# Kernel tuning notes

Measured on AMD Instinct MI355X. Metric: run time of the kernel, lower is better.

Reference implementation:

```python
import jax, jax.numpy as jnp
import numpy as np

B, L, D, H = 2, 2048, 1024, 16
LARGE_NEG = 10000.0
CLAMP = 20.0


def setup_inputs() -> dict:
    key = jax.random.key(0)
    ks = jax.random.split(key, 7)
    scale = 1.0 / np.sqrt(D)
    return {
        "x": jax.random.normal(ks[0], (B, L, D), dtype=jnp.float32),
        "key_padding_mask": jax.random.randint(ks[1], (B, L), 0, 2, dtype=jnp.int32),
        "attn_bias": jax.random.normal(ks[2], (B, H, L, L), dtype=jnp.float32),
        "W_in": jax.random.normal(ks[3], (3 * D, D), dtype=jnp.float32) * scale,
        "b_in": jnp.zeros((3 * D,), dtype=jnp.float32),
        "W_out": jax.random.normal(ks[4], (D, D), dtype=jnp.float32) * scale,
        "b_out": jnp.zeros((D,), dtype=jnp.float32),
    }


def reference(x, key_padding_mask, attn_bias, W_in, b_in, W_out, b_out):
    d = D // H
    # fused in-projection: [B,L,3D]
    qkv = x @ W_in.T + b_in
    q, k, v = jnp.split(qkv, 3, axis=-1)
    # [B,H,L,d]
    q = q.reshape(B, L, H, d).transpose(0, 2, 1, 3)
    k = k.reshape(B, L, H, d).transpose(0, 2, 1, 3)
    v = v.reshape(B, L, H, d).transpose(0, 2, 1, 3)
    scores = jnp.einsum("bhqd,bhkd->bhqk", q, k) / jnp.sqrt(jnp.float32(d))
    scores = scores + attn_bias
    # key padding: subtract large_neg where mask==1 (mask broadcast over heads, queries)
    pad = key_padding_mask.astype(scores.dtype)[:, None, None, :]
    scores = scores - LARGE_NEG * pad
    # stabilization + clamp before softmax (faithful to original)
    scores = scores - jnp.max(scores, axis=-1, keepdims=True)
    scores = jnp.clip(scores, -CLAMP, CLAMP)
    attn = jax.nn.softmax(scores, axis=-1)
    out = jnp.einsum("bhqk,bhkd->bhqd", attn, v)
    out = out.transpose(0, 2, 1, 3).reshape(B, L, D)
    return out @ W_out.T + b_out
```

## Files before the change

### kernel.cpp

```cpp
#include <hip/hip_runtime.h>
#include <hip/hip_bf16.h>
#include <cstddef>

#define Bdim 2
#define Ldim 2048
#define Ddim 1024
#define Hdim 16
#define HD   64

typedef __bf16 bf16;
typedef __bf16 bf16x8 __attribute__((ext_vector_type(8)));
typedef __bf16 bf16x4 __attribute__((ext_vector_type(4)));
typedef float  f32x4  __attribute__((ext_vector_type(4)));

__device__ __forceinline__ f32x4 zero4() { f32x4 z = {0.0f, 0.0f, 0.0f, 0.0f}; return z; }

__device__ __forceinline__ void load_lds16(const void* g, void* l) {
    __builtin_amdgcn_global_load_lds((__attribute__((address_space(1))) void*)g,
                                     (__attribute__((address_space(3))) void*)l,
                                     16, 0, 0);
}

__global__ __launch_bounds__(256) void cast_kernel(const float* __restrict__ in,
                                                   bf16* __restrict__ out, int n) {
    int i = (blockIdx.x * 256 + threadIdx.x) * 4;
    if (i >= n) return;
    float4 v = *(const float4*)(in + i);
    bf16x4 o;
    o[0] = (bf16)v.x; o[1] = (bf16)v.y; o[2] = (bf16)v.z; o[3] = (bf16)v.w;
    *(bf16x4*)(out + i) = o;
}

template<int MODE>
__global__ __launch_bounds__(256)
void gemm_nt(const bf16* __restrict__ A, const bf16* __restrict__ Bm,
             const float* __restrict__ bias, float* __restrict__ outF,
             bf16* __restrict__ qb, bf16* __restrict__ kb, bf16* __restrict__ vtmp,
             int M, int N, int K)
{
    __shared__ __align__(16) bf16 As[128 * 64];
    __shared__ __align__(16) bf16 Bs[128 * 64];
    const int tid  = threadIdx.x;
    const int wave = tid >> 6;
    const int lane = tid & 63;
    const int quad = lane >> 4;
    const int l16  = lane & 15;
    const int m0 = blockIdx.y * 128;
    const int n0 = blockIdx.x * 128;
    const int wm = (wave >> 1) * 64;
    const int wn = (wave & 1) * 64;

    f32x4 acc[4][4];
#pragma unroll
    for (int i = 0; i < 4; i++)
#pragma unroll
        for (int j = 0; j < 4; j++) acc[i][j] = zero4();

    const int srow = lane >> 3;
    const int scol = (lane & 7) * 8;

    for (int k0 = 0; k0 < K; k0 += 64) {
#pragma unroll
        for (int t = 0; t < 4; t++) {
            const int blk = wave * 4 + t;
            const int row = blk * 8 + srow;
            load_lds16(A  + (size_t)(m0 + row) * K + k0 + scol, As + blk * 512);
            load_lds16(Bm + (size_t)(n0 + row) * K + k0 + scol, Bs + blk * 512);
        }
        __syncthreads();
#pragma unroll
        for (int kk = 0; kk < 64; kk += 32) {
            bf16x8 af[4], bfr[4];
#pragma unroll
            for (int i = 0; i < 4; i++) {
                af[i]  = *(const bf16x8*)&As[(wm + i * 16 + l16) * 64 + kk + quad * 8];
                bfr[i] = *(const bf16x8*)&Bs[(wn + i * 16 + l16) * 64 + kk + quad * 8];
            }
#pragma unroll
            for (int i = 0; i < 4; i++)
#pragma unroll
                for (int j = 0; j < 4; j++)
                    acc[i][j] = __builtin_amdgcn_mfma_f32_16x16x32_bf16(af[i], bfr[j], acc[i][j], 0, 0, 0);
        }
        __syncthreads();
    }

#pragma unroll
    for (int i = 0; i < 4; i++)
#pragma unroll
        for (int j = 0; j < 4; j++)
#pragma unroll
            for (int r = 0; r < 4; r++) {
                const int gm = m0 + wm + i * 16 + quad * 4 + r;
                const int gn = n0 + wn + j * 16 + l16;
                float v = acc[i][j][r] + bias[gn];
                if (MODE == 0) {
                    const int bb = gm >> 11, ll = gm & (Ldim - 1);
                    const int seg = gn >> 10;
                    const int f = gn & 1023;
                    const int hh = f >> 6, dd = f & 63;
                    const size_t off = ((size_t)(bb * Hdim + hh) * Ldim + ll) * HD + dd;
                    const bf16 bv = (bf16)v;
                    if (seg == 0) qb[off] = bv;
                    else if (seg == 1) kb[off] = bv;
                    else vtmp[off] = bv;
                } else {
                    outF[(size_t)gm * N + gn] = v;
                }
            }
}

__global__ __launch_bounds__(256)
void transpose_v(const bf16* __restrict__ vtmp, bf16* __restrict__ vtb) {
    const int bh = blockIdx.x, lt = blockIdx.y;
    __shared__ bf16 T[64][65];
    const int tid = threadIdx.x;
#pragma unroll
    for (int i = 0; i < 16; i++) {
        int flat = i * 256 + tid;
        int r = flat >> 6, c = flat & 63;
        T[r][c] = vtmp[((size_t)bh * Ldim + lt * 64 + r) * HD + c];
    }
    __syncthreads();
#pragma unroll
    for (int i = 0; i < 16; i++) {
        int flat = i * 256 + tid;
        int dd = flat >> 6, ll = flat & 63;
        vtb[((size_t)bh * HD + dd) * Ldim + lt * 64 + ll] = T[ll][dd];
    }
}

__global__ __launch_bounds__(256)
void attn_kernel(const bf16* __restrict__ qb, const bf16* __restrict__ kb,
                 const bf16* __restrict__ vtb, const float* __restrict__ bias,
                 const int* __restrict__ pad, bf16* __restrict__ ob)
{
    const int bh = blockIdx.x;
    const int qt = blockIdx.y;
    const int b  = bh >> 4;
    const int h  = bh & 15;
    const int tid  = threadIdx.x;
    const int wave = tid >> 6, lane = tid & 63;
    const int quad = lane >> 4, l16 = lane & 15;

    __shared__ float padLDS[Ldim];
    __shared__ __align__(16) bf16 Ps[4][16][72];

    for (int i = tid; i < Ldim; i += 256)
        padLDS[i] = -10000.0f * (float)pad[b * Ldim + i];
    __syncthreads();

    const int qrow = qt * 64 + wave * 16 + l16;
    bf16x8 aq[2];
#pragma unroll
    for (int c = 0; c < 2; c++)
        aq[c] = *(const bf16x8*)&qb[((size_t)bh * Ldim + qrow) * HD + c * 32 + quad * 8];

    float mrow[4], lrow[4];
    f32x4 oacc[4];
#pragma unroll
    for (int r = 0; r < 4; r++) { mrow[r] = -1e30f; lrow[r] = 0.0f; }
#pragma unroll
    for (int j = 0; j < 4; j++) oacc[j] = zero4();

    const float scale = 0.125f;
    const int qbase = qt * 64 + wave * 16 + quad * 4;
    const int biasRow0 = ((b * Hdim + h) * Ldim + qbase) * Ldim;

    float bcur[4][4], bnxt[4][4];
#pragma unroll
    for (int j = 0; j < 4; j++)
#pragma unroll
        for (int r = 0; r < 4; r++)
            bcur[j][r] = bias[biasRow0 + r * Ldim + j * 16 + l16];

    for (int kt = 0; kt < Ldim; kt += 64) {
        const int ktn = (kt + 64 < Ldim) ? kt + 64 : kt;
#pragma unroll
        for (int j = 0; j < 4; j++)
#pragma unroll
            for (int r = 0; r < 4; r++)
                bnxt[j][r] = bias[biasRow0 + r * Ldim + ktn + j * 16 + l16];
        __builtin_amdgcn_sched_barrier(0);

        f32x4 s[4];
#pragma unroll
        for (int j = 0; j < 4; j++) {
            bf16x8 bk0 = *(const bf16x8*)&kb[((size_t)bh * Ldim + kt + j * 16 + l16) * HD + quad * 8];
            bf16x8 bk1 = *(const bf16x8*)&kb[((size_t)bh * Ldim + kt + j * 16 + l16) * HD + 32 + quad * 8];
            f32x4 t = __builtin_amdgcn_mfma_f32_16x16x32_bf16(aq[0], bk0, zero4(), 0, 0, 0);
            s[j]    = __builtin_amdgcn_mfma_f32_16x16x32_bf16(aq[1], bk1, t, 0, 0, 0);
        }
#pragma unroll
        for (int j = 0; j < 4; j++) {
            const int kcol = kt + j * 16 + l16;
            const float padv = padLDS[kcol];
#pragma unroll
            for (int r = 0; r < 4; r++)
                s[j][r] = s[j][r] * scale + bcur[j][r] + padv;
        }
        float alpha[4];
#pragma unroll
        for (int r = 0; r < 4; r++) {
            float v = fmaxf(fmaxf(s[0][r], s[1][r]), fmaxf(s[2][r], s[3][r]));
            v = fmaxf(v, __shfl_xor(v, 1));
            v = fmaxf(v, __shfl_xor(v, 2));
            v = fmaxf(v, __shfl_xor(v, 4));
            v = fmaxf(v, __shfl_xor(v, 8));
            const float mn = fmaxf(mrow[r], v);
            alpha[r] = __expf(mrow[r] - mn);
            mrow[r] = mn;
        }
        float rsum[4] = {0.0f, 0.0f, 0.0f, 0.0f};
#pragma unroll
        for (int j = 0; j < 4; j++)
#pragma unroll
            for (int r = 0; r < 4; r++) {
                float p = __expf(s[j][r] - mrow[r]);
                s[j][r] = p;
                rsum[r] += p;
            }
#pragma unroll
        for (int r = 0; r < 4; r++) {
            float v = rsum[r];
            v += __shfl_xor(v, 1); v += __shfl_xor(v, 2);
            v += __shfl_xor(v, 4); v += __shfl_xor(v, 8);
            lrow[r] = lrow[r] * alpha[r] + v;
        }
#pragma unroll
        for (int j = 0; j < 4; j++)
#pragma unroll
            for (int r = 0; r < 4; r++)
                Ps[wave][quad * 4 + r][j * 16 + l16] = (bf16)s[j][r];
#pragma unroll
        for (int j = 0; j < 4; j++)
#pragma unroll
            for (int r = 0; r < 4; r++)
                oacc[j][r] *= alpha[r];
#pragma unroll
        for (int c = 0; c < 2; c++) {
            bf16x8 ap = *(const bf16x8*)&Ps[wave][l16][c * 32 + quad * 8];
#pragma unroll
            for (int j = 0; j < 4; j++) {
                bf16x8 bv = *(const bf16x8*)&vtb[((size_t)bh * HD + j * 16 + l16) * Ldim + kt + c * 32 + quad * 8];
                oacc[j] = __builtin_amdgcn_mfma_f32_16x16x32_bf16(ap, bv, oacc[j], 0, 0, 0);
            }
        }
#pragma unroll
        for (int j = 0; j < 4; j++)
#pragma unroll
            for (int r = 0; r < 4; r++)
                bcur[j][r] = bnxt[j][r];
    }

#pragma unroll
    for (int r = 0; r < 4; r++) {
        const float inv = 1.0f / lrow[r];
        const int q = qbase + r;
#pragma unroll
        for (int j = 0; j < 4; j++) {
            float v = oacc[j][r] * inv;
            ob[((size_t)b * Ldim + q) * Ddim + h * HD + j * 16 + l16] = (bf16)v;
        }
    }
}

extern "C" void kernel_launch(void* const* d_in, const int* in_sizes, int n_in,
                              void* d_out, int out_size, void* d_ws, size_t ws_size,
                              hipStream_t stream) {
    const float* x     = (const float*)d_in[0];
    const int*   mask  = (const int*)  d_in[1];
    const float* bias  = (const float*)d_in[2];
    const float* W_in  = (const float*)d_in[3];
    const float* b_in  = (const float*)d_in[4];
    const float* W_out = (const float*)d_in[5];
    const float* b_out = (const float*)d_in[6];
    float* out = (float*)d_out;

    char* ws = (char*)d_ws;
    bf16* xb    = (bf16*)(ws);
    bf16* winb  = (bf16*)(ws + 8388608);
    bf16* woutb = (bf16*)(ws + 14680064);
    bf16* qb    = (bf16*)(ws + 16777216);
    bf16* kb    = (bf16*)(ws + 25165824);
    bf16* vtmp  = (bf16*)(ws + 33554432);
    bf16* vtb   = (bf16*)(ws + 41943040);
    bf16* ob    = xb;

    cast_kernel<<<4096, 256, 0, stream>>>(x,     xb,    Bdim * Ldim * Ddim);
    cast_kernel<<<3072, 256, 0, stream>>>(W_in,  winb,  3 * Ddim * Ddim);
    cast_kernel<<<1024, 256, 0, stream>>>(W_out, woutb, Ddim * Ddim);

    gemm_nt<0><<<dim3(24, 32), 256, 0, stream>>>(xb, winb, b_in, nullptr, qb, kb, vtmp,
                                                 Bdim * Ldim, 3 * Ddim, Ddim);
    transpose_v<<<dim3(32, 32), 256, 0, stream>>>(vtmp, vtb);
    attn_kernel<<<dim3(32, 32), 256, 0, stream>>>(qb, kb, vtb, bias, mask, ob);
    gemm_nt<1><<<dim3(8, 32), 256, 0, stream>>>(ob, woutb, b_out, out, nullptr, nullptr, nullptr,
                                                Bdim * Ldim, Ddim, Ddim);
}
```

Before: 1.030 ms.

## Double-buffer K/V tiles in swizzled LDS via async global-to-LDS loads

The attention kernel now stages each 64-key K tile and V^T tile into double-buffered, XOR-swizzled shared memory using global_load_lds. The next tile is prefetched while the current one is computed, so all four waves share K/V data instead of each re-reading it from global memory. The pad-mask LDS table is replaced by per-lane register prefetch, and the P staging buffer is swizzled to reduce bank conflicts. This adds a block-wide barrier per key tile, and there is a question of whether the async LDS writes are guaranteed visible before use without an explicit vmcnt wait.

```diff
diff --git a/kernel.cpp b/kernel.cpp
--- a/kernel.cpp
+++ b/kernel.cpp
@@ -143,12 +143,14 @@
     const int wave = tid >> 6, lane = tid & 63;
     const int quad = lane >> 4, l16 = lane & 15;
 
-    __shared__ float padLDS[Ldim];
-    __shared__ __align__(16) bf16 Ps[4][16][72];
-
-    for (int i = tid; i < Ldim; i += 256)
-        padLDS[i] = -10000.0f * (float)pad[b * Ldim + i];
-    __syncthreads();
+    __shared__ __align__(16) bf16 Ks[2][64 * 64];
+    __shared__ __align__(16) bf16 Vs[2][64 * 64];
+    __shared__ __align__(16) bf16 Ps[4][16 * 64];
+
+    const int srow = lane >> 3;
+    const int sgsw = ((lane & 7) ^ srow) << 3;
+    const bf16* kbase = kb  + (size_t)bh * Ldim * HD;
+    const bf16* vbase = vtb + (size_t)bh * HD * Ldim;
 
     const int qrow = qt * 64 + wave * 16 + l16;
     bf16x8 aq[2];
@@ -167,34 +169,54 @@
     const int qbase = qt * 64 + wave * 16 + quad * 4;
     const int biasRow0 = ((b * Hdim + h) * Ldim + qbase) * Ldim;
 
-    float bcur[4][4], bnxt[4][4];
-#pragma unroll
-    for (int j = 0; j < 4; j++)
+#pragma unroll
+    for (int c = 0; c < 2; c++) {
+        const int chunk = wave * 2 + c;
+        load_lds16(kbase + (size_t)(chunk * 8 + srow) * HD + sgsw, &Ks[0][chunk * 512]);
+        load_lds16(vbase + (size_t)(chunk * 8 + srow) * Ldim + sgsw, &Vs[0][chunk * 512]);
+    }
+    float bcur[4][4], bnxt[4][4], padc[4], padn[4];
+#pragma unroll
+    for (int j = 0; j < 4; j++) {
+        padc[j] = -10000.0f * (float)pad[b * Ldim + j * 16 + l16];
 #pragma unroll
         for (int r = 0; r < 4; r++)
             bcur[j][r] = bias[biasRow0 + r * Ldim + j * 16 + l16];
-
+    }
+    __syncthreads();
+
+    int cur = 0;
     for (int kt = 0; kt < Ldim; kt += 64) {
+        const int nxt = cur ^ 1;
         const int ktn = (kt + 64 < Ldim) ? kt + 64 : kt;
-#pragma unroll
-        for (int j = 0; j < 4; j++)
+
+#pragma unroll
+        for (int c = 0; c < 2; c++) {
+            const int chunk = wave * 2 + c;
+            load_lds16(kbase + (size_t)(ktn + chunk * 8 + srow) * HD + sgsw, &Ks[nxt][chunk * 512]);
+            load_lds16(vbase + (size_t)(chunk * 8 + srow) * Ldim + ktn + sgsw, &Vs[nxt][chunk * 512]);
+        }
+#pragma unroll
+        for (int j = 0; j < 4; j++) {
+            padn[j] = -10000.0f * (float)pad[b * Ldim + ktn + j * 16 + l16];
 #pragma unroll
             for (int r = 0; r < 4; r++)
                 bnxt[j][r] = bias[biasRow0 + r * Ldim + ktn + j * 16 + l16];
+        }
         __builtin_amdgcn_sched_barrier(0);
 
         f32x4 s[4];
 #pragma unroll
         for (int j = 0; j < 4; j++) {
-            bf16x8 bk0 = *(const bf16x8*)&kb[((size_t)bh * Ldim + kt + j * 16 + l16) * HD + quad * 8];
-            bf16x8 bk1 = *(const bf16x8*)&kb[((size_t)bh * Ldim + kt + j * 16 + l16) * HD + 32 + quad * 8];
+            const int krow = j * 16 + l16;
+            bf16x8 bk0 = *(const bf16x8*)&Ks[cur][krow * 64 + ((quad       ^ (l16 & 7)) << 3)];
+            bf16x8 bk1 = *(const bf16x8*)&Ks[cur][krow * 64 + (((4 + quad) ^ (l16 & 7)) << 3)];
             f32x4 t = __builtin_amdgcn_mfma_f32_16x16x32_bf16(aq[0], bk0, zero4(), 0, 0, 0);
             s[j]    = __builtin_amdgcn_mfma_f32_16x16x32_bf16(aq[1], bk1, t, 0, 0, 0);
         }
 #pragma unroll
         for (int j = 0; j < 4; j++) {
-            const int kcol = kt + j * 16 + l16;
-            const float padv = padLDS[kcol];
+            const float padv = padc[j];
 #pragma unroll
             for (int r = 0; r < 4; r++)
                 s[j][r] = s[j][r] * scale + bcur[j][r] + padv;
@@ -230,8 +252,11 @@
 #pragma unroll
         for (int j = 0; j < 4; j++)
 #pragma unroll
-            for (int r = 0; r < 4; r++)
-                Ps[wave][quad * 4 + r][j * 16 + l16] = (bf16)s[j][r];
+            for (int r = 0; r < 4; r++) {
+                const int row = quad * 4 + r;
+                const int g = (j * 2 + (l16 >> 3)) ^ (row & 7);
+                Ps[wave][row * 64 + g * 8 + (l16 & 7)] = (bf16)s[j][r];
+            }
 #pragma unroll
         for (int j = 0; j < 4; j++)
 #pragma unroll
@@ -239,18 +264,23 @@
                 oacc[j][r] *= alpha[r];
 #pragma unroll
         for (int c = 0; c < 2; c++) {
-            bf16x8 ap = *(const bf16x8*)&Ps[wave][l16][c * 32 + quad * 8];
+            const int gsw = ((c * 4 + quad) ^ (l16 & 7)) << 3;
+            bf16x8 ap = *(const bf16x8*)&Ps[wave][l16 * 64 + gsw];
 #pragma unroll
             for (int j = 0; j < 4; j++) {
-                bf16x8 bv = *(const bf16x8*)&vtb[((size_t)bh * HD + j * 16 + l16) * Ldim + kt + c * 32 + quad * 8];
+                bf16x8 bv = *(const bf16x8*)&Vs[cur][(j * 16 + l16) * 64 + gsw];
                 oacc[j] = __builtin_amdgcn_mfma_f32_16x16x32_bf16(ap, bv, oacc[j], 0, 0, 0);
             }
         }
-#pragma unroll
-        for (int j = 0; j < 4; j++)
+        __syncthreads();
+        cur = nxt;
+#pragma unroll
+        for (int j = 0; j < 4; j++) {
+            padc[j] = padn[j];
 #pragma unroll
             for (int r = 0; r < 4; r++)
                 bcur[j][r] = bnxt[j][r];
+        }
     }
 
 #pragma unroll
```

Result: faster. 904.9 us (-12.1%).
